# Performance work log

Hardware: AMD Instinct MI355X
Metric: run time of the kernel (lower is better)

## Reference

```python
import jax, jax.numpy as jnp
import numpy as np

DEPTH = 6
H = 12
D = 768
FF = 4 * D
OUT_INDICES = (2, 5)
EPS = 1e-5


def layernorm(x, g, b):
    m = jnp.mean(x, axis=-1, keepdims=True)
    v = jnp.mean(jnp.square(x - m), axis=-1, keepdims=True)
    return (x - m) * jax.lax.rsqrt(v + EPS) * g + b


def setup_inputs() -> dict:
    key = jax.random.key(0)
    ks = jax.random.split(key, 8)
    B, N = 2, 1024
    s = 0.02
    inp = {
        "x": jax.random.normal(ks[0], (B, N, D), dtype=jnp.float32),
        "rel_bias": jax.random.normal(ks[1], (H, N, N), dtype=jnp.float32),
        "ln1_g": jnp.ones((DEPTH, D), jnp.float32),
        "ln1_b": jnp.zeros((DEPTH, D), jnp.float32),
        "qkv_w": jax.random.normal(ks[2], (DEPTH, D, 3 * D), dtype=jnp.float32) * s,
        "out_w": jax.random.normal(ks[3], (DEPTH, D, D), dtype=jnp.float32) * s,
        "out_b": jnp.zeros((DEPTH, D), jnp.float32),
        "ln2_g": jnp.ones((DEPTH, D), jnp.float32),
        "ln2_b": jnp.zeros((DEPTH, D), jnp.float32),
        "ff1_w": jax.random.normal(ks[4], (DEPTH, D, FF), dtype=jnp.float32) * s,
        "ff1_b": jnp.zeros((DEPTH, FF), jnp.float32),
        "ff2_w": jax.random.normal(ks[5], (DEPTH, FF, D), dtype=jnp.float32) * s,
        "ff2_b": jnp.zeros((DEPTH, D), jnp.float32),
        "lnf_g": jnp.ones((D,), jnp.float32),
        "lnf_b": jnp.zeros((D,), jnp.float32),
    }
    return inp


def reference(x, rel_bias, ln1_g, ln1_b, qkv_w, out_w, out_b, ln2_g, ln2_b,
              ff1_w, ff1_b, ff2_w, ff2_b, lnf_g, lnf_b):
    B, N, Dm = x.shape
    Dh = Dm // H
    scale = Dh ** -0.5
    kside = int(round(N ** 0.5))  # N is a perfect square (patch grid)
    feats = []
    for i in range(DEPTH):
        # --- attention block ---
        h = layernorm(x, ln1_g[i], ln1_b[i])
        qkv = h @ qkv_w[i]                                   # [B,N,3D]
        q, k, v = jnp.split(qkv, 3, axis=-1)
        q = q.reshape(B, N, H, Dh).transpose(0, 2, 1, 3)     # [B,H,N,Dh]
        k = k.reshape(B, N, H, Dh).transpose(0, 2, 1, 3)
        v = v.reshape(B, N, H, Dh).transpose(0, 2, 1, 3)
        scores = jnp.einsum('bhid,bhjd->bhij', q, k) * scale + rel_bias
        attn = jax.nn.softmax(scores, axis=-1)
        o = jnp.einsum('bhij,bhjd->bhid', attn, v)
        o = o.transpose(0, 2, 1, 3).reshape(B, N, Dm)
        x = x + (o @ out_w[i] + out_b[i])
        # --- FFN block ---
        h2 = layernorm(x, ln2_g[i], ln2_b[i])
        ff = jax.nn.gelu(h2 @ ff1_w[i] + ff1_b[i], approximate=False)
        x = x + (ff @ ff2_w[i] + ff2_b[i])
        if i in OUT_INDICES:
            feats.append(x.reshape(B, kside, kside, Dm).transpose(0, 3, 1, 2))
    xf = layernorm(x, lnf_g, lnf_b)
    return (xf, *feats)
```

## Files before the change

### kernel.cpp

```cpp
#include <hip/hip_runtime.h>
#include <hip/hip_bf16.h>

typedef unsigned short ushort_t;
typedef __attribute__((ext_vector_type(8))) __bf16 bf16x8;
typedef __attribute__((ext_vector_type(4))) float f32x4;
typedef __attribute__((ext_vector_type(4))) unsigned int u32x4;

#define DEPTH 6
#define HEADS 12
#define DMODEL 768
#define FFDIM 3072
#define BATCH 2
#define SEQ 1024
#define ROWS (BATCH * SEQ)

static __device__ __forceinline__ ushort_t f2bf(float f) {
  unsigned u = __builtin_bit_cast(unsigned, f);
  u += 0x7fffu + ((u >> 16) & 1u);
  return (ushort_t)(u >> 16);
}

template <int MREP, int NREP, int EPI>
__global__ __launch_bounds__(256) void gemm_bt(
    const ushort_t* __restrict__ A, const ushort_t* __restrict__ Bt,
    int lda, int ldb, int K,
    void* __restrict__ out0, void* __restrict__ out1,
    const float* __restrict__ f0) {
  constexpr int BM = 32 * MREP;
  constexpr int BN = 32 * NREP;
  constexpr int CHA = BM / 32;
  constexpr int CHB = BN / 32;
  __shared__ ushort_t sA[2][BM * 64];
  __shared__ ushort_t sB[2][BN * 64];

  const int tid = threadIdx.x;
  const int lane = tid & 63;
  const int wid = tid >> 6;
  const int wm = wid >> 1, wn = wid & 1;

  int bx, by;
  {
    const int nb = gridDim.x * gridDim.y;
    const int bid = blockIdx.y * gridDim.x + blockIdx.x;
    const int q = nb >> 3;
    const int swz = (bid & 7) * q + (bid >> 3);
    bx = swz % gridDim.x;
    by = swz / gridDim.x;
  }

  const ushort_t* Ab = A + (long)bx * BM * lda;
  const ushort_t* Bb = Bt + (long)by * BN * ldb;

  const int srow = lane >> 3;
  const int scol = ((lane & 7) ^ srow) * 8;

  f32x4 acc[MREP][NREP];
#pragma unroll
  for (int m = 0; m < MREP; ++m)
#pragma unroll
    for (int n = 0; n < NREP; ++n) acc[m][n] = (f32x4){0.f, 0.f, 0.f, 0.f};

  const int fr = lane & 15;
  const int kq4 = lane >> 4;

  auto stage_tile = [&](int buf, int t) {
    const int k0 = t * 64;
#pragma unroll
    for (int j = 0; j < CHA; ++j) {
      const int c = wid * CHA + j;
      const ushort_t* src = Ab + (long)(c * 8 + srow) * lda + k0 + scol;
      __builtin_amdgcn_global_load_lds(
          (const __attribute__((address_space(1))) void*)src,
          (__attribute__((address_space(3))) void*)&sA[buf][c * 512], 16, 0, 0);
    }
#pragma unroll
    for (int j = 0; j < CHB; ++j) {
      const int c = wid * CHB + j;
      const ushort_t* src = Bb + (long)(c * 8 + srow) * ldb + k0 + scol;
      __builtin_amdgcn_global_load_lds(
          (const __attribute__((address_space(1))) void*)src,
          (__attribute__((address_space(3))) void*)&sB[buf][c * 512], 16, 0, 0);
    }
  };

  const int nt = K / 64;
  stage_tile(0, 0);
  for (int t = 0; t < nt; ++t) {
    const int cur = t & 1;
    asm volatile("s_waitcnt vmcnt(0)" ::: "memory");
    __builtin_amdgcn_s_barrier();
    if (t + 1 < nt) stage_tile(cur ^ 1, t + 1);
#pragma unroll
    for (int kk = 0; kk < 2; ++kk) {
      bf16x8 af[MREP], bfr[NREP];
#pragma unroll
      for (int m = 0; m < MREP; ++m) {
        const int row = wm * (MREP * 16) + m * 16 + fr;
        const int ch = (kk * 4 + kq4) ^ (row & 7);
        af[m] = *(const bf16x8*)&sA[cur][row * 64 + ch * 8];
      }
#pragma unroll
      for (int n = 0; n < NREP; ++n) {
        const int row = wn * (NREP * 16) + n * 16 + fr;
        const int ch = (kk * 4 + kq4) ^ (row & 7);
        bfr[n] = *(const bf16x8*)&sB[cur][row * 64 + ch * 8];
      }
#pragma unroll
      for (int m = 0; m < MREP; ++m)
#pragma unroll
        for (int n = 0; n < NREP; ++n)
          acc[m][n] = __builtin_amdgcn_mfma_f32_16x16x32_bf16(
              af[m], bfr[n], acc[m][n], 0, 0, 0);
    }
  }

  const long grow0 = (long)bx * BM + wm * (MREP * 16);
  const long gcol0 = (long)by * BN + wn * (NREP * 16);
  const int rr = (lane >> 4) * 4;
  const int cc = lane & 15;

#pragma unroll
  for (int m = 0; m < MREP; ++m) {
#pragma unroll
    for (int n = 0; n < NREP; ++n) {
#pragma unroll
      for (int r = 0; r < 4; ++r) {
        long row = grow0 + m * 16 + rr + r;
        long col = gcol0 + n * 16 + cc;
        float c = acc[m][n][r];
        if (EPI == 0) {
          ushort_t bv = f2bf(c);
          if (col < 1536) {
            ((ushort_t*)out0)[row * 2304 + col] = bv;
          } else {
            long h = (col - 1536) >> 6, d = (col - 1536) & 63;
            long b = row >> 10, i = row & 1023;
            ((ushort_t*)out1)[(((b * HEADS) + h) * 64 + d) * 1024 + i] = bv;
          }
        } else if (EPI == 3) {
          long idx = row * DMODEL + col;
          ((float*)out0)[idx] += c + f0[col];
        } else if (EPI == 4) {
          float t = c + f0[col];
          float g = 0.5f * t * (1.0f + erff(t * 0.70710678118f));
          ((ushort_t*)out0)[row * FFDIM + col] = f2bf(g);
        } else if (EPI == 5) {
          long idx = row * DMODEL + col;
          ((float*)out0)[idx] += c + f0[col];
        }
      }
    }
  }
}

__global__ __launch_bounds__(256) void flash_attn(
    const ushort_t* __restrict__ qkv,
    const ushort_t* __restrict__ vt,
    const float* __restrict__ rel,
    ushort_t* __restrict__ o) {
  __shared__ ushort_t sK[2][64 * 64];
  __shared__ ushort_t sV[2][64 * 64];
  __shared__ ushort_t sP[64 * 64];

  const int tid = threadIdx.x;
  const int lane = tid & 63;
  const int wid = tid >> 6;
  const int h = blockIdx.y, b = blockIdx.z;
  const int q0 = blockIdx.x * 64;

  const int fr = lane & 15;
  const int kq4 = lane >> 4;
  const int rr = kq4 * 4;
  const int cc = fr;

  const int srow = lane >> 3;
  const int scol = ((lane & 7) ^ srow) * 8;

  const ushort_t* qbase =
      qkv + (size_t)(b * 1024 + q0 + wid * 16 + fr) * 2304 + h * 64;
  bf16x8 qreg[2];
  qreg[0] = *(const bf16x8*)&qbase[kq4 * 8];
  qreg[1] = *(const bf16x8*)&qbase[32 + kq4 * 8];

  const ushort_t* Kbase = qkv + (size_t)(b * 1024) * 2304 + 768 + h * 64;
  const ushort_t* Vbase = vt + (size_t)((b * HEADS + h) * 64) * 1024;

  f32x4 acc_o[4];
  float m_run[4], l_run[4];
#pragma unroll
  for (int n = 0; n < 4; ++n) acc_o[n] = (f32x4){0.f, 0.f, 0.f, 0.f};
#pragma unroll
  for (int r = 0; r < 4; ++r) { m_run[r] = -1e30f; l_run[r] = 0.f; }

  auto stage_kv = [&](int buf, int t) {
#pragma unroll
    for (int j = 0; j < 2; ++j) {
      const int c = wid * 2 + j;
      const ushort_t* src = Kbase + (size_t)(t * 64 + c * 8 + srow) * 2304 + scol;
      __builtin_amdgcn_global_load_lds(
          (const __attribute__((address_space(1))) void*)src,
          (__attribute__((address_space(3))) void*)&sK[buf][c * 512], 16, 0, 0);
    }
#pragma unroll
    for (int j = 0; j < 2; ++j) {
      const int c = wid * 2 + j;
      const ushort_t* src = Vbase + (size_t)(c * 8 + srow) * 1024 + t * 64 + scol;
      __builtin_amdgcn_global_load_lds(
          (const __attribute__((address_space(1))) void*)src,
          (__attribute__((address_space(3))) void*)&sV[buf][c * 512], 16, 0, 0);
    }
  };

  stage_kv(0, 0);
  for (int t = 0; t < 16; ++t) {
    const int cur = t & 1;
    asm volatile("s_waitcnt vmcnt(0)" ::: "memory");
    __builtin_amdgcn_s_barrier();

    float bias[4][4];
    {
      const float* rb = rel + ((size_t)h << 20) +
                        (size_t)(q0 + wid * 16 + rr) * 1024 + t * 64 + cc;
#pragma unroll
      for (int n = 0; n < 4; ++n)
#pragma unroll
        for (int r = 0; r < 4; ++r) bias[n][r] = rb[(size_t)r * 1024 + n * 16];
    }

    if (t + 1 < 16) stage_kv(cur ^ 1, t + 1);

    f32x4 s[4];
#pragma unroll
    for (int n = 0; n < 4; ++n) s[n] = (f32x4){0.f, 0.f, 0.f, 0.f};
#pragma unroll
    for (int kk = 0; kk < 2; ++kk) {
#pragma unroll
      for (int n = 0; n < 4; ++n) {
        const int row = n * 16 + fr;
        const int ch = (kk * 4 + kq4) ^ (row & 7);
        bf16x8 kf = *(const bf16x8*)&sK[cur][row * 64 + ch * 8];
        s[n] =
            __builtin_amdgcn_mfma_f32_16x16x32_bf16(qreg[kk], kf, s[n], 0, 0, 0);
      }
    }

    float mr[4];
#pragma unroll
    for (int r = 0; r < 4; ++r) mr[r] = -1e30f;
#pragma unroll
    for (int n = 0; n < 4; ++n)
#pragma unroll
      for (int r = 0; r < 4; ++r) {
        float v = s[n][r] * 0.125f + bias[n][r];
        s[n][r] = v;
        mr[r] = fmaxf(mr[r], v);
      }
#pragma unroll
    for (int o_ = 1; o_ < 16; o_ <<= 1)
#pragma unroll
      for (int r = 0; r < 4; ++r) mr[r] = fmaxf(mr[r], __shfl_xor(mr[r], o_));

    float escale[4], psum[4];
#pragma unroll
    for (int r = 0; r < 4; ++r) {
      float mn = fmaxf(m_run[r], mr[r]);
      escale[r] = __expf(m_run[r] - mn);
      m_run[r] = mn;
      psum[r] = 0.f;
    }
#pragma unroll
    for (int n = 0; n < 4; ++n)
#pragma unroll
      for (int r = 0; r < 4; ++r) {
        float p = __expf(s[n][r] - m_run[r]);
        psum[r] += p;
        const int prow = wid * 16 + rr + r;
        const int pcol = n * 16 + cc;
        sP[prow * 64 + (((pcol >> 3) ^ (prow & 7)) << 3) + (pcol & 7)] = f2bf(p);
      }
#pragma unroll
    for (int o_ = 1; o_ < 16; o_ <<= 1)
#pragma unroll
      for (int r = 0; r < 4; ++r) psum[r] += __shfl_xor(psum[r], o_);
#pragma unroll
    for (int r = 0; r < 4; ++r) l_run[r] = l_run[r] * escale[r] + psum[r];

    asm volatile("s_waitcnt lgkmcnt(0)" ::: "memory");
    __builtin_amdgcn_s_barrier();

#pragma unroll
    for (int n = 0; n < 4; ++n)
#pragma unroll
      for (int r = 0; r < 4; ++r) acc_o[n][r] *= escale[r];
#pragma unroll
    for (int kk = 0; kk < 2; ++kk) {
      const int prow = wid * 16 + fr;
      const int pch = (kk * 4 + kq4) ^ (prow & 7);
      bf16x8 pf = *(const bf16x8*)&sP[prow * 64 + pch * 8];
#pragma unroll
      for (int n = 0; n < 4; ++n) {
        const int vrow = n * 16 + fr;
        const int vch = (kk * 4 + kq4) ^ (vrow & 7);
        bf16x8 vf = *(const bf16x8*)&sV[cur][vrow * 64 + vch * 8];
        acc_o[n] =
            __builtin_amdgcn_mfma_f32_16x16x32_bf16(pf, vf, acc_o[n], 0, 0, 0);
      }
    }
  }

  ushort_t* ob = o + (size_t)(b * 1024 + q0 + wid * 16) * 768 + h * 64;
#pragma unroll
  for (int r = 0; r < 4; ++r) {
    const float rinv = 1.f / l_run[r];
#pragma unroll
    for (int n = 0; n < 4; ++n)
      ob[(size_t)(rr + r) * 768 + n * 16 + cc] = f2bf(acc_o[n][r] * rinv);
  }
}

__global__ __launch_bounds__(256) void transpose_cast(
    const float* __restrict__ in, ushort_t* __restrict__ out, int R, int C) {
  __shared__ float t[32][33];
  const float* ip = in + (long)blockIdx.z * R * C;
  ushort_t* op = out + (long)blockIdx.z * R * C;
  int c0 = blockIdx.x * 32, r0 = blockIdx.y * 32;
  int tx = threadIdx.x;
  for (int i = threadIdx.y; i < 32; i += 8)
    t[i][tx] = ip[(long)(r0 + i) * C + c0 + tx];
  __syncthreads();
  for (int i = threadIdx.y; i < 32; i += 8)
    op[(long)(c0 + i) * R + r0 + tx] = f2bf(t[tx][i]);
}

__global__ __launch_bounds__(256) void ln_kernel(
    const float* __restrict__ x, const float* __restrict__ g,
    const float* __restrict__ b, void* __restrict__ out, int out_f32) {
  int row = blockIdx.x;
  int tid = threadIdx.x;
  int lane = tid & 63, wid = tid >> 6;
  const float* xr = x + (long)row * DMODEL;
  float v0 = xr[tid], v1 = xr[tid + 256], v2 = xr[tid + 512];
  float s = v0 + v1 + v2;
  __shared__ float red[8];
  for (int o = 32; o; o >>= 1) s += __shfl_xor(s, o);
  if (!lane) red[wid] = s;
  __syncthreads();
  float mean = (red[0] + red[1] + red[2] + red[3]) * (1.f / 768.f);
  float d0 = v0 - mean, d1 = v1 - mean, d2 = v2 - mean;
  float q = d0 * d0 + d1 * d1 + d2 * d2;
  for (int o = 32; o; o >>= 1) q += __shfl_xor(q, o);
  if (!lane) red[4 + wid] = q;
  __syncthreads();
  float var = (red[4] + red[5] + red[6] + red[7]) * (1.f / 768.f);
  float rs = rsqrtf(var + 1e-5f);
  float y0 = d0 * rs * g[tid] + b[tid];
  float y1 = d1 * rs * g[tid + 256] + b[tid + 256];
  float y2 = d2 * rs * g[tid + 512] + b[tid + 512];
  if (out_f32) {
    float* o_ = (float*)out + (long)row * DMODEL;
    o_[tid] = y0; o_[tid + 256] = y1; o_[tid + 512] = y2;
  } else {
    ushort_t* o_ = (ushort_t*)out + (long)row * DMODEL;
    o_[tid] = f2bf(y0); o_[tid + 256] = f2bf(y1); o_[tid + 512] = f2bf(y2);
  }
}

__global__ __launch_bounds__(256) void feat_kernel(const float* __restrict__ x,
                                                   float* __restrict__ out) {
  __shared__ float t[32][33];
  const float* xp = x + (long)blockIdx.z * SEQ * DMODEL;
  float* op = out + (long)blockIdx.z * DMODEL * SEQ;
  int n0 = blockIdx.x * 32, c0 = blockIdx.y * 32;
  int tx = threadIdx.x;
  for (int i = threadIdx.y; i < 32; i += 8)
    t[i][tx] = xp[(long)(n0 + i) * DMODEL + c0 + tx];
  __syncthreads();
  for (int i = threadIdx.y; i < 32; i += 8)
    op[(long)(c0 + i) * SEQ + n0 + tx] = t[tx][i];
}

extern "C" void kernel_launch(void* const* d_in, const int* in_sizes, int n_in,
                              void* d_out, int out_size, void* d_ws,
                              size_t ws_size, hipStream_t stream) {
  const float* x_in   = (const float*)d_in[0];
  const float* rel    = (const float*)d_in[1];
  const float* ln1_g  = (const float*)d_in[2];
  const float* ln1_b  = (const float*)d_in[3];
  const float* qkv_w  = (const float*)d_in[4];
  const float* out_w  = (const float*)d_in[5];
  const float* out_b  = (const float*)d_in[6];
  const float* ln2_g  = (const float*)d_in[7];
  const float* ln2_b  = (const float*)d_in[8];
  const float* ff1_w  = (const float*)d_in[9];
  const float* ff1_b  = (const float*)d_in[10];
  const float* ff2_w  = (const float*)d_in[11];
  const float* ff2_b  = (const float*)d_in[12];
  const float* lnf_g  = (const float*)d_in[13];
  const float* lnf_b  = (const float*)d_in[14];
  float* out = (float*)d_out;

  char* w = (char*)d_ws;
  ushort_t* wq_t = (ushort_t*)w; w += (size_t)DEPTH * 2304 * 768 * 2;
  ushort_t* wo_t = (ushort_t*)w; w += (size_t)DEPTH * 768 * 768 * 2;
  ushort_t* wf1_t = (ushort_t*)w; w += (size_t)DEPTH * 3072 * 768 * 2;
  ushort_t* wf2_t = (ushort_t*)w; w += (size_t)DEPTH * 768 * 3072 * 2;
  float* xb = (float*)w; w += (size_t)ROWS * DMODEL * 4;
  ushort_t* hb = (ushort_t*)w; w += (size_t)ROWS * DMODEL * 2;
  ushort_t* qkvb = (ushort_t*)w; w += (size_t)ROWS * 2304 * 2;
  ushort_t* vt = (ushort_t*)w; w += (size_t)BATCH * HEADS * 64 * 1024 * 2;
  ushort_t* ob = (ushort_t*)w; w += (size_t)ROWS * DMODEL * 2;
  ushort_t* ffb = (ushort_t*)w; w += (size_t)ROWS * FFDIM * 2;

  dim3 tb(32, 8);
  transpose_cast<<<dim3(2304 / 32, 768 / 32, DEPTH), tb, 0, stream>>>(
      qkv_w, wq_t, 768, 2304);
  transpose_cast<<<dim3(768 / 32, 768 / 32, DEPTH), tb, 0, stream>>>(
      out_w, wo_t, 768, 768);
  transpose_cast<<<dim3(3072 / 32, 768 / 32, DEPTH), tb, 0, stream>>>(
      ff1_w, wf1_t, 768, 3072);
  transpose_cast<<<dim3(768 / 32, 3072 / 32, DEPTH), tb, 0, stream>>>(
      ff2_w, wf2_t, 3072, 768);

  hipMemcpyAsync(xb, x_in, (size_t)ROWS * DMODEL * 4, hipMemcpyDeviceToDevice,
                 stream);

  for (int i = 0; i < DEPTH; ++i) {
    ln_kernel<<<ROWS, 256, 0, stream>>>(xb, ln1_g + i * 768, ln1_b + i * 768,
                                        hb, 0);
    gemm_bt<2, 2, 0><<<dim3(32, 36), 256, 0, stream>>>(
        hb, wq_t + (size_t)i * 2304 * 768, 768, 768, 768, qkvb, vt, nullptr);
    flash_attn<<<dim3(16, HEADS, BATCH), 256, 0, stream>>>(qkvb, vt, rel, ob);
    gemm_bt<1, 2, 3><<<dim3(64, 12), 256, 0, stream>>>(
        ob, wo_t + (size_t)i * 768 * 768, 768, 768, 768, xb, nullptr,
        out_b + i * 768);
    ln_kernel<<<ROWS, 256, 0, stream>>>(xb, ln2_g + i * 768, ln2_b + i * 768,
                                        hb, 0);
    gemm_bt<2, 2, 4><<<dim3(32, 48), 256, 0, stream>>>(
        hb, wf1_t + (size_t)i * 3072 * 768, 768, 768, 768, ffb, nullptr,
        ff1_b + i * 3072);
    gemm_bt<1, 2, 5><<<dim3(64, 12), 256, 0, stream>>>(
        ffb, wf2_t + (size_t)i * 768 * 3072, 3072, 3072, 3072, xb, nullptr,
        ff2_b + i * 768);
    if (i == 2)
      feat_kernel<<<dim3(32, 24, 2), tb, 0, stream>>>(xb, out + 1572864);
    if (i == 5)
      feat_kernel<<<dim3(32, 24, 2), tb, 0, stream>>>(xb, out + 2 * 1572864);
  }
  ln_kernel<<<ROWS, 256, 0, stream>>>(xb, lnf_g, lnf_b, out, 1);
}
```

Before: 927.2 us.

## Pre-pack relative bias to bf16 fragment layout and shrink attention blocks

Adds a one-time kernel per call that converts the fp32 relative-position bias into bf16, reordered so that each lane's 16 bias values for a 16x64 tile sit contiguously. Flash attention then reads them with two 16-byte vector loads, prefetched one tile ahead, instead of sixteen strided fp32 scalar loads. This halves bias bandwidth across the six layers. Blocks shrink to 2 waves over 32 query rows with doubled grid, giving more blocks per head but more K/V restaging; bias rounding to bf16 adds small numeric error.

```diff
diff --git a/kernel.cpp b/kernel.cpp
--- a/kernel.cpp
+++ b/kernel.cpp
@@ -3,6 +3,7 @@
 
 typedef unsigned short ushort_t;
 typedef __attribute__((ext_vector_type(8))) __bf16 bf16x8;
+typedef __attribute__((ext_vector_type(8))) unsigned short u16x8;
 typedef __attribute__((ext_vector_type(4))) float f32x4;
 typedef __attribute__((ext_vector_type(4))) unsigned int u32x4;
 
@@ -18,6 +19,9 @@
   unsigned u = __builtin_bit_cast(unsigned, f);
   u += 0x7fffu + ((u >> 16) & 1u);
   return (ushort_t)(u >> 16);
+}
+static __device__ __forceinline__ float bf2f(ushort_t v) {
+  return __builtin_bit_cast(float, (unsigned)v << 16);
 }
 
 template <int MREP, int NREP, int EPI>
@@ -153,20 +157,43 @@
   }
 }
 
-__global__ __launch_bounds__(256) void flash_attn(
+__global__ __launch_bounds__(256) void pack_bias(const float* __restrict__ rel,
+                                                 ushort_t* __restrict__ pb) {
+  __shared__ ushort_t tile[1024];
+  const int blk = blockIdx.x;
+  const int t = blk & 15, qi = (blk >> 4) & 63, h = blk >> 10;
+  const float* src = rel + ((size_t)h << 20) + (size_t)(qi * 16) * 1024 + t * 64;
+  const int tid = threadIdx.x;
+  const int kk = tid & 63;
+#pragma unroll
+  for (int it = 0; it < 4; ++it) {
+    const int qr = (tid >> 6) * 4 + it;
+    const float v = src[(size_t)qr * 1024 + kk];
+    const int lane = (qr >> 2) * 16 + (kk & 15);
+    const int idx = (kk >> 4) * 4 + (qr & 3);
+    tile[lane * 16 + idx] = f2bf(v);
+  }
+  __syncthreads();
+  ushort_t* dst = pb + (size_t)blk * 1024;
+#pragma unroll
+  for (int it = 0; it < 4; ++it) dst[it * 256 + tid] = tile[it * 256 + tid];
+}
+
+__global__ __launch_bounds__(128) void flash_attn(
     const ushort_t* __restrict__ qkv,
     const ushort_t* __restrict__ vt,
-    const float* __restrict__ rel,
+    const ushort_t* __restrict__ pbias,
     ushort_t* __restrict__ o) {
   __shared__ ushort_t sK[2][64 * 64];
   __shared__ ushort_t sV[2][64 * 64];
-  __shared__ ushort_t sP[64 * 64];
+  __shared__ ushort_t sP[32 * 64];
 
   const int tid = threadIdx.x;
   const int lane = tid & 63;
   const int wid = tid >> 6;
   const int h = blockIdx.y, b = blockIdx.z;
-  const int q0 = blockIdx.x * 64;
+  const int q0 = blockIdx.x * 32;
+  const int qi = blockIdx.x * 2 + wid;
 
   const int fr = lane & 15;
   const int kq4 = lane >> 4;
@@ -184,6 +211,7 @@
 
   const ushort_t* Kbase = qkv + (size_t)(b * 1024) * 2304 + 768 + h * 64;
   const ushort_t* Vbase = vt + (size_t)((b * HEADS + h) * 64) * 1024;
+  const ushort_t* pbb = pbias + (((size_t)h * 64 + qi) << 14) + lane * 16;
 
   f32x4 acc_o[4];
   float m_run[4], l_run[4];
@@ -194,16 +222,16 @@
 
   auto stage_kv = [&](int buf, int t) {
 #pragma unroll
-    for (int j = 0; j < 2; ++j) {
-      const int c = wid * 2 + j;
+    for (int j = 0; j < 4; ++j) {
+      const int c = wid * 4 + j;
       const ushort_t* src = Kbase + (size_t)(t * 64 + c * 8 + srow) * 2304 + scol;
       __builtin_amdgcn_global_load_lds(
           (const __attribute__((address_space(1))) void*)src,
           (__attribute__((address_space(3))) void*)&sK[buf][c * 512], 16, 0, 0);
     }
 #pragma unroll
-    for (int j = 0; j < 2; ++j) {
-      const int c = wid * 2 + j;
+    for (int j = 0; j < 4; ++j) {
+      const int c = wid * 4 + j;
       const ushort_t* src = Vbase + (size_t)(c * 8 + srow) * 1024 + t * 64 + scol;
       __builtin_amdgcn_global_load_lds(
           (const __attribute__((address_space(1))) void*)src,
@@ -211,23 +239,16 @@
     }
   };
 
-  stage_kv(0, 0);
-  for (int t = 0; t < 16; ++t) {
+  auto step = [&](int t, u16x8& bc0, u16x8& bc1, u16x8& bn0, u16x8& bn1) {
     const int cur = t & 1;
     asm volatile("s_waitcnt vmcnt(0)" ::: "memory");
     __builtin_amdgcn_s_barrier();
-
-    float bias[4][4];
-    {
-      const float* rb = rel + ((size_t)h << 20) +
-                        (size_t)(q0 + wid * 16 + rr) * 1024 + t * 64 + cc;
-#pragma unroll
-      for (int n = 0; n < 4; ++n)
-#pragma unroll
-        for (int r = 0; r < 4; ++r) bias[n][r] = rb[(size_t)r * 1024 + n * 16];
-    }
-
-    if (t + 1 < 16) stage_kv(cur ^ 1, t + 1);
+    if (t + 1 < 16) {
+      stage_kv(cur ^ 1, t + 1);
+      const ushort_t* pp = pbb + (size_t)(t + 1) * 1024;
+      bn0 = *(const u16x8*)pp;
+      bn1 = *(const u16x8*)(pp + 8);
+    }
 
     f32x4 s[4];
 #pragma unroll
@@ -251,7 +272,9 @@
     for (int n = 0; n < 4; ++n)
 #pragma unroll
       for (int r = 0; r < 4; ++r) {
-        float v = s[n][r] * 0.125f + bias[n][r];
+        const int idx = n * 4 + r;
+        const float bv = bf2f(idx < 8 ? bc0[idx] : bc1[idx - 8]);
+        float v = s[n][r] * 0.125f + bv;
         s[n][r] = v;
         mr[r] = fmaxf(mr[r], v);
       }
@@ -306,6 +329,15 @@
             __builtin_amdgcn_mfma_f32_16x16x32_bf16(pf, vf, acc_o[n], 0, 0, 0);
       }
     }
+  };
+
+  u16x8 bA0, bA1, bB0, bB1;
+  bA0 = *(const u16x8*)pbb;
+  bA1 = *(const u16x8*)(pbb + 8);
+  stage_kv(0, 0);
+  for (int tt = 0; tt < 16; tt += 2) {
+    step(tt, bA0, bA1, bB0, bB1);
+    step(tt + 1, bB0, bB1, bA0, bA1);
   }
 
   ushort_t* ob = o + (size_t)(b * 1024 + q0 + wid * 16) * 768 + h * 64;
@@ -410,6 +442,7 @@
   ushort_t* vt = (ushort_t*)w; w += (size_t)BATCH * HEADS * 64 * 1024 * 2;
   ushort_t* ob = (ushort_t*)w; w += (size_t)ROWS * DMODEL * 2;
   ushort_t* ffb = (ushort_t*)w; w += (size_t)ROWS * FFDIM * 2;
+  ushort_t* pbias = (ushort_t*)w; w += (size_t)HEADS * 1024 * 1024 * 2;
 
   dim3 tb(32, 8);
   transpose_cast<<<dim3(2304 / 32, 768 / 32, DEPTH), tb, 0, stream>>>(
@@ -420,6 +453,7 @@
       ff1_w, wf1_t, 768, 3072);
   transpose_cast<<<dim3(768 / 32, 3072 / 32, DEPTH), tb, 0, stream>>>(
       ff2_w, wf2_t, 3072, 768);
+  pack_bias<<<HEADS * 64 * 16, 256, 0, stream>>>(rel, pbias);
 
   hipMemcpyAsync(xb, x_in, (size_t)ROWS * DMODEL * 4, hipMemcpyDeviceToDevice,
                  stream);
@@ -429,7 +463,7 @@
                                         hb, 0);
     gemm_bt<2, 2, 0><<<dim3(32, 36), 256, 0, stream>>>(
         hb, wq_t + (size_t)i * 2304 * 768, 768, 768, 768, qkvb, vt, nullptr);
-    flash_attn<<<dim3(16, HEADS, BATCH), 256, 0, stream>>>(qkvb, vt, rel, ob);
+    flash_attn<<<dim3(32, HEADS, BATCH), 128, 0, stream>>>(qkvb, vt, pbias, ob);
     gemm_bt<1, 2, 3><<<dim3(64, 12), 256, 0, stream>>>(
         ob, wo_t + (size_t)i * 768 * 768, 768, 768, 768, xb, nullptr,
         out_b + i * 768);
```

Result: no change. 928.0 us (median of 2 runs) (+0.1%).
